# Kernel tuning notes

Measured on AMD Instinct MI355X. Metric: run time of the kernel, lower is better.

Reference implementation:

```python
import jax, jax.numpy as jnp
import numpy as np

BS, NQ, NV, E = 8, 1000, 20000, 256
HH, DH, L, P, FFN = 8, 32, 1, 4, 512
SPATIAL = ((100, 200),)  # (H, W) per level; sum(H*W) == NV


def layer_norm(x, w, b):
    mu = jnp.mean(x, -1, keepdims=True)
    var = jnp.mean((x - mu) ** 2, -1, keepdims=True)
    return (x - mu) / jnp.sqrt(var + 1e-5) * w + b


def mha(q_in, k_in, v_in, in_w, in_b, out_w, out_b):
    # q_in/k_in/v_in: (len, BS, E), batch_first=False semantics of nn.MultiheadAttention
    Wq, Wk, Wv = jnp.split(in_w, 3, axis=0)
    bq, bk, bv = jnp.split(in_b, 3, axis=0)
    def heads(x, W, b):  # (len,B,E) -> (B,HH,len,DH)
        y = x @ W.T + b
        return y.reshape(y.shape[0], BS, HH, DH).transpose(1, 2, 0, 3)
    q = heads(q_in, Wq, bq) / jnp.sqrt(jnp.asarray(DH, q_in.dtype))
    k = heads(k_in, Wk, bk)
    v = heads(v_in, Wv, bv)
    attn = jax.nn.softmax(jnp.einsum('bhqd,bhkd->bhqk', q, k), axis=-1)
    o = jnp.einsum('bhqk,bhkd->bhqd', attn, v)  # (B,HH,Lq,DH)
    o = o.transpose(2, 0, 1, 3).reshape(-1, BS, E)
    return o @ out_w.T + out_b


def bilinear_sample(img, grid):
    # img: (B,H,W,C); grid: (B,NQ,P,2) in [-1,1]; align_corners=False, zero padding
    B, H, W, C = img.shape
    x = (grid[..., 0] + 1.0) * 0.5 * W - 0.5
    y = (grid[..., 1] + 1.0) * 0.5 * H - 0.5
    x0 = jnp.floor(x); y0 = jnp.floor(y)
    wx = x - x0; wy = y - y0
    flat = img.reshape(B, H * W, C)
    def gather(xi, yi):
        valid = (xi >= 0) & (xi < W) & (yi >= 0) & (yi < H)
        xc = jnp.clip(xi, 0, W - 1).astype(jnp.int32)
        yc = jnp.clip(yi, 0, H - 1).astype(jnp.int32)
        idx = (yc * W + xc).reshape(B, -1, 1)
        v = jnp.take_along_axis(flat, idx, axis=1).reshape(*xi.shape, C)
        return v * valid[..., None].astype(img.dtype)
    v00 = gather(x0, y0); v01 = gather(x0 + 1, y0)
    v10 = gather(x0, y0 + 1); v11 = gather(x0 + 1, y0 + 1)
    wx = wx[..., None]; wy = wy[..., None]
    return (v00 * (1 - wx) * (1 - wy) + v01 * wx * (1 - wy)
            + v10 * (1 - wx) * wy + v11 * wx * wy)


def msda(value, sampling_locations, attention_weights):
    # value: (BS,NV,HH,DH); locations: (BS,NQ,HH,L,P,2); weights: (BS,NQ,HH,L,P)
    grids = 2.0 * sampling_locations - 1.0
    start = 0
    outs = []
    for lvl, (H, W) in enumerate(SPATIAL):
        v = value[:, start:start + H * W]           # (BS,HW,HH,DH)
        start += H * W
        img = v.transpose(0, 2, 1, 3).reshape(BS * HH, H, W, DH)
        g = grids[:, :, :, lvl].transpose(0, 2, 1, 3, 4).reshape(BS * HH, NQ, P, 2)
        outs.append(bilinear_sample(img, g))        # (BS*HH,NQ,P,DH)
    sampled = jnp.stack(outs, axis=2)               # (BS*HH,NQ,L,P,DH)
    aw = attention_weights.transpose(0, 2, 1, 3, 4).reshape(BS * HH, NQ, L, P)
    out = jnp.einsum('bqlpd,bqlp->bqd', sampled, aw)
    return out.reshape(BS, HH, NQ, DH).transpose(0, 2, 1, 3).reshape(BS, NQ, E)


def setup_inputs() -> dict:
    key = jax.random.key(0)
    ks = jax.random.split(key, 24)
    s = 1.0 / np.sqrt(E)
    # sampling_offsets bias: torch init grid (circular directions scaled by point idx)
    th = np.arange(HH, dtype=np.float32) * (2.0 * np.pi / HH)
    grid = np.stack([np.cos(th), np.sin(th)], -1)
    grid = grid / np.abs(grid).max(-1, keepdims=True)
    grid = np.tile(grid[:, None, None, :], (1, L, P, 1)) * np.arange(1, P + 1, dtype=np.float32)[None, None, :, None]
    return {
        'query': jax.random.normal(ks[0], (NQ, BS, E), jnp.float32),
        'query_pos': jax.random.normal(ks[1], (NQ, BS, E), jnp.float32),
        'value': jax.random.normal(ks[2], (NV, BS, E), jnp.float32),
        'reference_points': jax.random.uniform(ks[3], (BS, NQ, L, 2), jnp.float32),
        'in_proj_w': jax.random.normal(ks[4], (3 * E, E), jnp.float32) * s,
        'in_proj_b': jnp.zeros((3 * E,), jnp.float32),
        'out_proj_w': jax.random.normal(ks[5], (E, E), jnp.float32) * s,
        'out_proj_b': jnp.zeros((E,), jnp.float32),
        'ln1_w': jnp.ones((E,), jnp.float32), 'ln1_b': jnp.zeros((E,), jnp.float32),
        'ln2_w': jnp.ones((E,), jnp.float32), 'ln2_b': jnp.zeros((E,), jnp.float32),
        'ln3_w': jnp.ones((E,), jnp.float32), 'ln3_b': jnp.zeros((E,), jnp.float32),
        'off_w': jax.random.normal(ks[6], (HH * L * P * 2, E), jnp.float32) * 0.01,
        'off_b': jnp.asarray(grid.reshape(-1)),
        'aw_w': jax.random.normal(ks[7], (HH * L * P, E), jnp.float32) * 0.01,
        'aw_b': jnp.zeros((HH * L * P,), jnp.float32),
        'vproj_w': jax.random.normal(ks[8], (E, E), jnp.float32) * s,
        'vproj_b': jnp.zeros((E,), jnp.float32),
        'oproj_w': jax.random.normal(ks[9], (E, E), jnp.float32) * s,
        'oproj_b': jnp.zeros((E,), jnp.float32),
        'ffn_w1': jax.random.normal(ks[10], (FFN, E), jnp.float32) * s,
        'ffn_b1': jnp.zeros((FFN,), jnp.float32),
        'ffn_w2': jax.random.normal(ks[11], (E, FFN), jnp.float32) / np.sqrt(FFN),
        'ffn_b2': jnp.zeros((E,), jnp.float32),
    }


def reference(query, query_pos, value, reference_points,
              in_proj_w, in_proj_b, out_proj_w, out_proj_b,
              ln1_w, ln1_b, ln2_w, ln2_b, ln3_w, ln3_b,
              off_w, off_b, aw_w, aw_b, vproj_w, vproj_b, oproj_w, oproj_b,
              ffn_w1, ffn_b1, ffn_w2, ffn_b2):
    # --- self-attn: q=k=query+pos, v=query; residual inside; dropout=eval (identity)
    qp = query + query_pos
    x = layer_norm(query + mha(qp, qp, query, in_proj_w, in_proj_b, out_proj_w, out_proj_b), ln1_w, ln1_b)
    # --- deformable cross-attn ---
    xq_b = (x + query_pos).transpose(1, 0, 2)         # (BS,NQ,E)
    v = (value.transpose(1, 0, 2) @ vproj_w.T + vproj_b).reshape(BS, NV, HH, DH)
    off = (xq_b @ off_w.T + off_b).reshape(BS, NQ, HH, L, P, 2)
    aw = jax.nn.softmax((xq_b @ aw_w.T + aw_b).reshape(BS, NQ, HH, L * P), -1).reshape(BS, NQ, HH, L, P)
    norm = jnp.asarray([[w, h] for (h, w) in SPATIAL], jnp.float32)  # (L,2) = (W,H)
    loc = reference_points[:, :, None, :, None, :] + off / norm[None, None, None, :, None, :]
    ms = msda(v, loc, aw) @ oproj_w.T + oproj_b       # (BS,NQ,E)
    x = layer_norm(x + ms.transpose(1, 0, 2), ln2_w, ln2_b)
    # --- FFN ---
    h = jnp.maximum(x @ ffn_w1.T + ffn_b1, 0.0)
    return layer_norm(x + h @ ffn_w2.T + ffn_b2, ln3_w, ln3_b)
```

## Files before the change

### kernel.cpp

```cpp
#include <hip/hip_runtime.h>
#include <hip/hip_bf16.h>
#include <cmath>

constexpr int cBS = 8;
constexpr int cNQ = 1000;
constexpr int cNV = 20000;
constexpr int cE  = 256;
constexpr int cHH = 8;
constexpr int cDH = 32;
constexpr int cP  = 4;
constexpr int cFFN = 512;
constexpr int cH = 100;
constexpr int cW = 200;
constexpr int NTOK = cNQ * cBS;
constexpr size_t QKSZ2 = (size_t)64 * 1024 * cDH;

typedef float f32x4 __attribute__((ext_vector_type(4)));
typedef short bf16x8 __attribute__((ext_vector_type(8)));
union U8 { uint u[4]; bf16x8 v; };

__device__ __forceinline__ void split_bf(float x, ushort& h, ushort& l) {
    __hip_bfloat16 hb = __float2bfloat16(x);
    float hf = __bfloat162float(hb);
    __hip_bfloat16 lb = __float2bfloat16(x - hf);
    h = *reinterpret_cast<ushort*>(&hb);
    l = *reinterpret_cast<ushort*>(&lb);
}
__device__ __forceinline__ void pk_split2(float a, float b, uint& h, uint& l) {
    __hip_bfloat16 ah = __float2bfloat16(a), bh = __float2bfloat16(b);
    float arf = a - __bfloat162float(ah), brf = b - __bfloat162float(bh);
    __hip_bfloat16 al = __float2bfloat16(arf), bl = __float2bfloat16(brf);
    h = ((uint)*reinterpret_cast<ushort*>(&bh) << 16) | *reinterpret_cast<ushort*>(&ah);
    l = ((uint)*reinterpret_cast<ushort*>(&bl) << 16) | *reinterpret_cast<ushort*>(&al);
}

__global__ __launch_bounds__(256) void k_zerou4(uint4* __restrict__ p, int n)
{
    int i = blockIdx.x * 256 + threadIdx.x;
    if (i < n) p[i] = uint4{0u, 0u, 0u, 0u};
}

__global__ __launch_bounds__(256) void k_prepw(
    const float* __restrict__ Wsrc, ushort* __restrict__ wpk,
    int nkk , int total , int losz )
{
    int gid = blockIdx.x * 256 + threadIdx.x;
    if (gid >= total) return;
    int g  = gid & 3;
    int kk = (gid >> 2) % nkk;
    int n  = gid / (4 * nkk);
    const float* src = Wsrc + (size_t)n * (nkk * 32) + kk * 32 + 4 * g;
    float4 x0 = *reinterpret_cast<const float4*>(src);
    float4 x1 = *reinterpret_cast<const float4*>(src + 16);
    float xs[8] = {x0.x, x0.y, x0.z, x0.w, x1.x, x1.y, x1.z, x1.w};
    union { ushort s[8]; uint4 q; } hi_, lo_;
#pragma unroll
    for (int j = 0; j < 8; j++) split_bf(xs[j], hi_.s[j], lo_.s[j]);
    *reinterpret_cast<uint4*>(wpk + (size_t)gid * 8)        = hi_.q;
    *reinterpret_cast<uint4*>(wpk + losz + (size_t)gid * 8) = lo_.q;
}

__global__ __launch_bounds__(256) void k_prepw2(
    const float* __restrict__ Wsrc, ushort* __restrict__ wpk)
{
    int gid = blockIdx.x * 256 + threadIdx.x;
    if (gid >= 8192) return;
    int lane = gid & 63;
    int kk   = (gid >> 6) & 7;
    int nblk = gid >> 9;
    int ln = lane & 15, g = lane >> 4;
    const float* src = Wsrc + (size_t)(nblk * 16 + ln) * cE + kk * 32 + 4 * g;
    float4 x0 = *reinterpret_cast<const float4*>(src);
    float4 x1 = *reinterpret_cast<const float4*>(src + 16);
    float xs[8] = {x0.x, x0.y, x0.z, x0.w, x1.x, x1.y, x1.z, x1.w};
    union { ushort s[8]; uint4 q; } hi_, lo_;
#pragma unroll
    for (int j = 0; j < 8; j++) split_bf(xs[j], hi_.s[j], lo_.s[j]);
    *reinterpret_cast<uint4*>(wpk + (size_t)gid * 8)         = hi_.q;
    *reinterpret_cast<uint4*>(wpk + 65536 + (size_t)gid * 8) = lo_.q;
}

__global__ __launch_bounds__(256) void k_bgemm2(
    const float* __restrict__ A, const ushort* __restrict__ wpk2,
    const float* __restrict__ bias, float* __restrict__ vimg)
{
    __shared__ float lds[64][36];
    const int t    = threadIdx.x;
    const int w    = t >> 6;
    const int lane = t & 63;
    const int g    = lane >> 4;
    const int ln   = lane & 15;
    const int bm   = blockIdx.x * 64;
    const ushort* wlo = wpk2 + 65536;

    f32x4 acc[4][4];
#pragma unroll
    for (int mt = 0; mt < 4; mt++)
#pragma unroll
        for (int nt = 0; nt < 4; nt++) acc[mt][nt] = {0.f, 0.f, 0.f, 0.f};

    const int srow = t >> 2;
    const int scg  = (t & 3) * 8;

    for (int kk = 0; kk < 8; kk++) {
        {
            const float* src = A + (size_t)(bm + srow) * cE + kk * 32 + scg;
            float4 u0 = *reinterpret_cast<const float4*>(src);
            float4 u1 = *reinterpret_cast<const float4*>(src + 4);
            *reinterpret_cast<float4*>(&lds[srow][scg])     = u0;
            *reinterpret_cast<float4*>(&lds[srow][scg + 4]) = u1;
        }
        __syncthreads();

        U8 wh[4], wl[4];
#pragma unroll
        for (int nt = 0; nt < 4; nt++) {
            size_t off = (((size_t)(w * 4 + nt) * 8 + kk) * 64 + lane) * 8;
            *reinterpret_cast<uint4*>(&wh[nt].u[0]) = *reinterpret_cast<const uint4*>(wpk2 + off);
            *reinterpret_cast<uint4*>(&wl[nt].u[0]) = *reinterpret_cast<const uint4*>(wlo + off);
        }

#pragma unroll
        for (int mt = 0; mt < 4; mt++) {
            int row = mt * 16 + ln;
            float4 x0 = *reinterpret_cast<const float4*>(&lds[row][4 * g]);
            float4 x1 = *reinterpret_cast<const float4*>(&lds[row][16 + 4 * g]);
            float xs[8] = {x0.x, x0.y, x0.z, x0.w, x1.x, x1.y, x1.z, x1.w};
            U8 aH, aL;
            union { ushort s[8]; uint u[4]; } hs, ls;
#pragma unroll
            for (int j = 0; j < 8; j++) split_bf(xs[j], hs.s[j], ls.s[j]);
#pragma unroll
            for (int i = 0; i < 4; i++) { aH.u[i] = hs.u[i]; aL.u[i] = ls.u[i]; }
#pragma unroll
            for (int nt = 0; nt < 4; nt++) {
                acc[mt][nt] = __builtin_amdgcn_mfma_f32_16x16x32_bf16(aL.v, wh[nt].v, acc[mt][nt], 0, 0, 0);
                acc[mt][nt] = __builtin_amdgcn_mfma_f32_16x16x32_bf16(aH.v, wl[nt].v, acc[mt][nt], 0, 0, 0);
                acc[mt][nt] = __builtin_amdgcn_mfma_f32_16x16x32_bf16(aH.v, wh[nt].v, acc[mt][nt], 0, 0, 0);
            }
        }
        __syncthreads();
    }

#pragma unroll
    for (int nt = 0; nt < 4; nt++) {
        int n = w * 64 + nt * 16 + ln;
        float bv = bias[n];
#pragma unroll
        for (int mt = 0; mt < 4; mt++) {
#pragma unroll
            for (int r = 0; r < 4; r++) {
                int gr = bm + mt * 16 + 4 * g + r;
                vimg[(size_t)gr * cE + n] = acc[mt][nt][r] + bv;
            }
        }
    }
}

__global__ __launch_bounds__(256) void k_oagemm(
    const float* __restrict__ xq, const ushort* __restrict__ wpk,
    float* __restrict__ raw)
{
    const int w    = threadIdx.x >> 6;
    const int lane = threadIdx.x & 63;
    const int g    = lane >> 4;
    const int ln   = lane & 15;
    const int row0 = blockIdx.x * 64 + w * 16;
    const ushort* wlo = wpk + 24576;

    f32x4 acc[6];
#pragma unroll
    for (int nt = 0; nt < 6; nt++) acc[nt] = {0.f, 0.f, 0.f, 0.f};

    for (int kk = 0; kk < 8; kk++) {
        const float* ap = xq + (size_t)(row0 + ln) * cE + kk * 32 + 4 * g;
        float4 u0 = *reinterpret_cast<const float4*>(ap);
        float4 u1 = *reinterpret_cast<const float4*>(ap + 16);
        float xs[8] = {u0.x, u0.y, u0.z, u0.w, u1.x, u1.y, u1.z, u1.w};
        U8 aH, aL;
        union { ushort s[8]; uint u[4]; } hs, ls;
#pragma unroll
        for (int j = 0; j < 8; j++) split_bf(xs[j], hs.s[j], ls.s[j]);
#pragma unroll
        for (int i = 0; i < 4; i++) { aH.u[i] = hs.u[i]; aL.u[i] = ls.u[i]; }
#pragma unroll
        for (int nt = 0; nt < 6; nt++) {
            int n = nt * 16 + ln;
            size_t off = ((size_t)(n * 8 + kk) * 4 + g) * 8;
            U8 wh, wl;
            *reinterpret_cast<uint4*>(&wh.u[0]) = *reinterpret_cast<const uint4*>(wpk + off);
            *reinterpret_cast<uint4*>(&wl.u[0]) = *reinterpret_cast<const uint4*>(wlo + off);
            acc[nt] = __builtin_amdgcn_mfma_f32_16x16x32_bf16(aL.v, wh.v, acc[nt], 0, 0, 0);
            acc[nt] = __builtin_amdgcn_mfma_f32_16x16x32_bf16(aH.v, wl.v, acc[nt], 0, 0, 0);
            acc[nt] = __builtin_amdgcn_mfma_f32_16x16x32_bf16(aH.v, wh.v, acc[nt], 0, 0, 0);
        }
    }

#pragma unroll
    for (int nt = 0; nt < 6; nt++) {
        int n = nt * 16 + ln;
#pragma unroll
        for (int r = 0; r < 4; r++) {
            int row = row0 + 4 * g + r;
            raw[(size_t)row * 96 + n] = acc[nt][r];
        }
    }
}

__global__ __launch_bounds__(256) void k_locaw(
    const float* __restrict__ raw, const float* __restrict__ offb,
    const float* __restrict__ awbias, const float* __restrict__ refp,
    float* __restrict__ locO, float* __restrict__ awO)
{
    int gid = blockIdx.x * 256 + threadIdx.x;
    if (gid >= NTOK * 96) return;
    int i = gid % 96;
    int tok = gid / 96;
    int q = tok >> 3, b = tok & 7;
    int bq = b * cNQ + q;
    const float* rr = raw + (size_t)tok * 96;
    if (i < 64) {
        int c = i & 1;
        float offv = rr[i] + offb[i];
        float refv = refp[((size_t)b * cNQ + q) * 2 + c];
        float nrm = (c == 0) ? 200.f : 100.f;
        locO[(size_t)bq * 64 + i] = refv + offv / nrm;
    } else {
        int j = i - 64;
        int gbase = j & ~3;
        float x0 = rr[64 + gbase + 0] + awbias[gbase + 0];
        float x1 = rr[64 + gbase + 1] + awbias[gbase + 1];
        float x2 = rr[64 + gbase + 2] + awbias[gbase + 2];
        float x3 = rr[64 + gbase + 3] + awbias[gbase + 3];
        float xm = rr[64 + j] + awbias[j];
        float mx = fmaxf(fmaxf(x0, x1), fmaxf(x2, x3));
        float e = __expf(xm - mx);
        float ssum = __expf(x0 - mx) + __expf(x1 - mx) + __expf(x2 - mx) + __expf(x3 - mx);
        awO[(size_t)bq * 32 + j] = e / ssum;
    }
}

constexpr int MM_QKV   = 1;
constexpr int MM_PLAIN = 2;
constexpr int MM_RELU  = 3;
constexpr int MM_OPROJ = 4;

template <int MODE, int TKK, int NFULL>
__global__ __launch_bounds__(256) void k_mgemm(
    const float* __restrict__ A, const float* __restrict__ A2,
    const ushort* __restrict__ wpk, int losz,
    const float* __restrict__ bias,
    void* __restrict__ C0, void* __restrict__ C1, void* __restrict__ C2)
{
    const int w    = threadIdx.x >> 6;
    const int lane = threadIdx.x & 63;
    const int g    = lane >> 4;
    const int ln   = lane & 15;
    const int bm   = blockIdx.x * 32;
    const int slab = blockIdx.y;
    const int nb   = slab * 256 + w * 64;
    const ushort* wlo = wpk + losz;
    const int K = TKK * 32;

    f32x4 acc[2][4];
#pragma unroll
    for (int mt = 0; mt < 2; mt++)
#pragma unroll
        for (int nt = 0; nt < 4; nt++) acc[mt][nt] = {0.f, 0.f, 0.f, 0.f};

    U8 wh[2][4], wl[2][4];
    float ax[2][2][8];

#define MG_LOADW(kk, buf) {                                                        \
    _Pragma("unroll")                                                              \
    for (int nt = 0; nt < 4; nt++) {                                               \
        int n = nb + nt * 16 + ln;                                                 \
        size_t off = ((size_t)(n * TKK + (kk)) * 4 + g) * 8;                       \
        *reinterpret_cast<uint4*>(&wh[buf][nt].u[0]) = *reinterpret_cast<const uint4*>(wpk + off); \
        *reinterpret_cast<uint4*>(&wl[buf][nt].u[0]) = *reinterpret_cast<const uint4*>(wlo + off); \
    } }

#define MG_LOADA(kk, buf) {                                                        \
    _Pragma("unroll")                                                              \
    for (int mt = 0; mt < 2; mt++) {                                               \
        const float* ap = A + (size_t)(bm + mt * 16 + ln) * K + (kk) * 32 + 4 * g; \
        float4 u0 = *reinterpret_cast<const float4*>(ap);                          \
        float4 u1 = *reinterpret_cast<const float4*>(ap + 16);                     \
        if (MODE == MM_QKV && slab < 2) {                                          \
            const float* bp = A2 + (size_t)(bm + mt * 16 + ln) * K + (kk) * 32 + 4 * g; \
            float4 v0 = *reinterpret_cast<const float4*>(bp);                      \
            float4 v1 = *reinterpret_cast<const float4*>(bp + 16);                 \
            u0.x += v0.x; u0.y += v0.y; u0.z += v0.z; u0.w += v0.w;                \
            u1.x += v1.x; u1.y += v1.y; u1.z += v1.z; u1.w += v1.w;                \
        }                                                                          \
        ax[buf][mt][0] = u0.x; ax[buf][mt][1] = u0.y;                              \
        ax[buf][mt][2] = u0.z; ax[buf][mt][3] = u0.w;                              \
        ax[buf][mt][4] = u1.x; ax[buf][mt][5] = u1.y;                              \
        ax[buf][mt][6] = u1.z; ax[buf][mt][7] = u1.w;                              \
    } }

#define MG_STEP(buf) {                                                             \
    _Pragma("unroll")                                                              \
    for (int mt = 0; mt < 2; mt++) {                                               \
        U8 aH, aL;                                                                 \
        union { ushort s[8]; uint u[4]; } hs, ls;                                  \
        _Pragma("unroll")                                                          \
        for (int j = 0; j < 8; j++) split_bf(ax[buf][mt][j], hs.s[j], ls.s[j]);    \
        _Pragma("unroll")                                                          \
        for (int i = 0; i < 4; i++) { aH.u[i] = hs.u[i]; aL.u[i] = ls.u[i]; }      \
        _Pragma("unroll")                                                          \
        for (int nt = 0; nt < 4; nt++) {                                           \
            acc[mt][nt] = __builtin_amdgcn_mfma_f32_16x16x32_bf16(aL.v, wh[buf][nt].v, acc[mt][nt], 0, 0, 0); \
            acc[mt][nt] = __builtin_amdgcn_mfma_f32_16x16x32_bf16(aH.v, wl[buf][nt].v, acc[mt][nt], 0, 0, 0); \
            acc[mt][nt] = __builtin_amdgcn_mfma_f32_16x16x32_bf16(aH.v, wh[buf][nt].v, acc[mt][nt], 0, 0, 0); \
        }                                                                          \
    } }

    MG_LOADW(0, 0)
    MG_LOADA(0, 0)
#pragma unroll
    for (int kk = 0; kk < TKK; kk++) {
        if (kk + 1 < TKK) {
            MG_LOADW(kk + 1, (kk + 1) & 1)
            MG_LOADA(kk + 1, (kk + 1) & 1)
        }
        MG_STEP(kk & 1)
    }
#undef MG_LOADW
#undef MG_LOADA
#undef MG_STEP

#pragma unroll
    for (int nt = 0; nt < 4; nt++) {
        int n = nb + nt * 16 + ln;
        float bv = bias[n];
#pragma unroll
        for (int mt = 0; mt < 2; mt++) {
#pragma unroll
            for (int r = 0; r < 4; r++) {
                int gr = bm + mt * 16 + 4 * g + r;
                float val = acc[mt][nt][r] + bv;
                if (MODE == MM_QKV) {
                    int tok = gr >> 3, b = gr & 7;
                    int nloc = n & 255, h = nloc >> 5, d = nloc & 31;
                    if (slab == 0) val *= 0.17677669529663687f;
                    ushort hs, ls;
                    split_bf(val, hs, ls);
                    if (slab < 2) {
                        int slot = ((d >> 2) & 3) * 8 + (d & 3) + 4 * (d >> 4);
                        ushort* base = (slab == 0) ? (ushort*)C0 : (ushort*)C1;
                        size_t off = ((size_t)(b * cHH + h) * 1024 + tok) * 32 + slot;
                        base[off]         = hs;
                        base[QKSZ2 + off] = ls;
                    } else {
                        int o = tok & 31, kbi = tok >> 5;
                        int slot = ((o >> 2) & 3) * 8 + (o & 3) + 4 * (o >> 4);
                        ushort* vb = (ushort*)C2;
                        size_t off = ((size_t)(b * cHH + h) * 32 + d) * 1024 + kbi * 32 + slot;
                        vb[off]         = hs;
                        vb[QKSZ2 + off] = ls;
                    }
                } else if (MODE == MM_OPROJ) {
                    int b = gr / cNQ, q = gr - b * cNQ;
                    ((float*)C0)[((size_t)q * cBS + b) * cE + n] = val;
                } else {
                    if (MODE == MM_RELU) val = fmaxf(val, 0.f);
                    ((float*)C0)[(size_t)gr * NFULL + n] = val;
                }
            }
        }
    }
}

__global__ __launch_bounds__(256) void k_attn3(
    const ushort* __restrict__ qhi, const ushort* __restrict__ qlo,
    const ushort* __restrict__ khi, const ushort* __restrict__ klo,
    const ushort* __restrict__ vhi, const ushort* __restrict__ vlo,
    float* __restrict__ po, float* __restrict__ plsum)
{
    const int bid   = blockIdx.x;
    const int xcd   = bid & 7;
    const int inner = bid >> 3;
    const int bh    = ((inner & 7) << 3) + xcd;
    const int rest  = inner >> 3;
    const int qbix  = rest & 7;
    const int z     = rest >> 3;

    const int w    = threadIdx.x >> 6;
    const int lane = threadIdx.x & 63;
    const int g    = lane >> 4;
    const int ql   = lane & 15;
    const int qA   = qbix * 128 + w * 32;

    const size_t qoffA = ((size_t)bh * 1024 + qA + ql) * 32 + g * 8;
    U8 bQAh, bQAl, bQBh, bQBl;
    *reinterpret_cast<uint4*>(&bQAh.u[0]) = *reinterpret_cast<const uint4*>(qhi + qoffA);
    *reinterpret_cast<uint4*>(&bQAl.u[0]) = *reinterpret_cast<const uint4*>(qlo + qoffA);
    *reinterpret_cast<uint4*>(&bQBh.u[0]) = *reinterpret_cast<const uint4*>(qhi + qoffA + 16 * 32);
    *reinterpret_cast<uint4*>(&bQBl.u[0]) = *reinterpret_cast<const uint4*>(qlo + qoffA + 16 * 32);
    const size_t koff = ((size_t)bh * 1024 + ql) * 32 + g * 8;
    const size_t voff = ((size_t)bh * 32 + ql) * 1024 + g * 8;

    f32x4 oA0 = {0.f,0.f,0.f,0.f}, oA1 = {0.f,0.f,0.f,0.f};
    f32x4 oB0 = {0.f,0.f,0.f,0.f}, oB1 = {0.f,0.f,0.f,0.f};
    float lpartA = 0.f, lpartB = 0.f;
    const f32x4 zz = {0.f, 0.f, 0.f, 0.f};

    const int kt0 = z * 16;
#pragma unroll
    for (int kti = 0; kti < 16; kti++) {
        const int kt = kt0 + kti;
        U8 k0h, k1h, k0l, k1l, v0h, v1h, v0l, v1l;
        {
            size_t kb32 = (size_t)kt * 32 * 32;
            *reinterpret_cast<uint4*>(&k0h.u[0]) = *reinterpret_cast<const uint4*>(khi + koff + kb32);
            *reinterpret_cast<uint4*>(&k1h.u[0]) = *reinterpret_cast<const uint4*>(khi + koff + kb32 + 512);
            *reinterpret_cast<uint4*>(&k0l.u[0]) = *reinterpret_cast<const uint4*>(klo + koff + kb32);
            *reinterpret_cast<uint4*>(&k1l.u[0]) = *reinterpret_cast<const uint4*>(klo + koff + kb32 + 512);
            size_t vb32 = voff + (size_t)kt * 32;
            *reinterpret_cast<uint4*>(&v0h.u[0]) = *reinterpret_cast<const uint4*>(vhi + vb32);
            *reinterpret_cast<uint4*>(&v1h.u[0]) = *reinterpret_cast<const uint4*>(vhi + vb32 + 16 * 1024);
            *reinterpret_cast<uint4*>(&v0l.u[0]) = *reinterpret_cast<const uint4*>(vlo + vb32);
            *reinterpret_cast<uint4*>(&v1l.u[0]) = *reinterpret_cast<const uint4*>(vlo + vb32 + 16 * 1024);
        }

        const bool tail = (kti == 15) && (z == 1);

        f32x4 sA0 = __builtin_amdgcn_mfma_f32_16x16x32_bf16(k0l.v, bQAh.v, zz, 0, 0, 0);
        sA0 = __builtin_amdgcn_mfma_f32_16x16x32_bf16(k0h.v, bQAl.v, sA0, 0, 0, 0);
        sA0 = __builtin_amdgcn_mfma_f32_16x16x32_bf16(k0h.v, bQAh.v, sA0, 0, 0, 0);
        f32x4 sB0 = __builtin_amdgcn_mfma_f32_16x16x32_bf16(k0l.v, bQBh.v, zz, 0, 0, 0);
        sB0 = __builtin_amdgcn_mfma_f32_16x16x32_bf16(k0h.v, bQBl.v, sB0, 0, 0, 0);
        sB0 = __builtin_amdgcn_mfma_f32_16x16x32_bf16(k0h.v, bQBh.v, sB0, 0, 0, 0);
        f32x4 sA1, sB1;
        if (tail) {
            int tb = 31 * 32 + 4 * g;
#pragma unroll
            for (int r = 0; r < 4; r++) {
                if (tb + r >= cNQ) { sA0[r] = -INFINITY; sB0[r] = -INFINITY; }
            }
            sA1[0] = sA1[1] = sA1[2] = sA1[3] = -INFINITY;
            sB1[0] = sB1[1] = sB1[2] = sB1[3] = -INFINITY;
        } else {
            sA1 = __builtin_amdgcn_mfma_f32_16x16x32_bf16(k1l.v, bQAh.v, zz, 0, 0, 0);
            sA1 = __builtin_amdgcn_mfma_f32_16x16x32_bf16(k1h.v, bQAl.v, sA1, 0, 0, 0);
            sA1 = __builtin_amdgcn_mfma_f32_16x16x32_bf16(k1h.v, bQAh.v, sA1, 0, 0, 0);
            sB1 = __builtin_amdgcn_mfma_f32_16x16x32_bf16(k1l.v, bQBh.v, zz, 0, 0, 0);
            sB1 = __builtin_amdgcn_mfma_f32_16x16x32_bf16(k1h.v, bQBl.v, sB1, 0, 0, 0);
            sB1 = __builtin_amdgcn_mfma_f32_16x16x32_bf16(k1h.v, bQBh.v, sB1, 0, 0, 0);
        }

        float pA00 = __expf(sA0[0]), pA01 = __expf(sA0[1]);
        float pA02 = __expf(sA0[2]), pA03 = __expf(sA0[3]);
        float pA10 = __expf(sA1[0]), pA11 = __expf(sA1[1]);
        float pA12 = __expf(sA1[2]), pA13 = __expf(sA1[3]);
        lpartA += ((pA00 + pA01) + (pA02 + pA03)) + ((pA10 + pA11) + (pA12 + pA13));
        float pB00 = __expf(sB0[0]), pB01 = __expf(sB0[1]);
        float pB02 = __expf(sB0[2]), pB03 = __expf(sB0[3]);
        float pB10 = __expf(sB1[0]), pB11 = __expf(sB1[1]);
        float pB12 = __expf(sB1[2]), pB13 = __expf(sB1[3]);
        lpartB += ((pB00 + pB01) + (pB02 + pB03)) + ((pB10 + pB11) + (pB12 + pB13));

        U8 fpAh, fpAl, fpBh, fpBl;
        pk_split2(pA00, pA01, fpAh.u[0], fpAl.u[0]);
        pk_split2(pA02, pA03, fpAh.u[1], fpAl.u[1]);
        pk_split2(pA10, pA11, fpAh.u[2], fpAl.u[2]);
        pk_split2(pA12, pA13, fpAh.u[3], fpAl.u[3]);
        pk_split2(pB00, pB01, fpBh.u[0], fpBl.u[0]);
        pk_split2(pB02, pB03, fpBh.u[1], fpBl.u[1]);
        pk_split2(pB10, pB11, fpBh.u[2], fpBl.u[2]);
        pk_split2(pB12, pB13, fpBh.u[3], fpBl.u[3]);

        oA0 = __builtin_amdgcn_mfma_f32_16x16x32_bf16(v0l.v, fpAh.v, oA0, 0, 0, 0);
        oA0 = __builtin_amdgcn_mfma_f32_16x16x32_bf16(v0h.v, fpAl.v, oA0, 0, 0, 0);
        oA0 = __builtin_amdgcn_mfma_f32_16x16x32_bf16(v0h.v, fpAh.v, oA0, 0, 0, 0);
        oA1 = __builtin_amdgcn_mfma_f32_16x16x32_bf16(v1l.v, fpAh.v, oA1, 0, 0, 0);
        oA1 = __builtin_amdgcn_mfma_f32_16x16x32_bf16(v1h.v, fpAl.v, oA1, 0, 0, 0);
        oA1 = __builtin_amdgcn_mfma_f32_16x16x32_bf16(v1h.v, fpAh.v, oA1, 0, 0, 0);
        oB0 = __builtin_amdgcn_mfma_f32_16x16x32_bf16(v0l.v, fpBh.v, oB0, 0, 0, 0);
        oB0 = __builtin_amdgcn_mfma_f32_16x16x32_bf16(v0h.v, fpBl.v, oB0, 0, 0, 0);
        oB0 = __builtin_amdgcn_mfma_f32_16x16x32_bf16(v0h.v, fpBh.v, oB0, 0, 0, 0);
        oB1 = __builtin_amdgcn_mfma_f32_16x16x32_bf16(v1l.v, fpBh.v, oB1, 0, 0, 0);
        oB1 = __builtin_amdgcn_mfma_f32_16x16x32_bf16(v1h.v, fpBl.v, oB1, 0, 0, 0);
        oB1 = __builtin_amdgcn_mfma_f32_16x16x32_bf16(v1h.v, fpBh.v, oB1, 0, 0, 0);
    }

    float lsumA = lpartA;
    lsumA += __shfl_xor(lsumA, 16, 64);
    lsumA += __shfl_xor(lsumA, 32, 64);
    float lsumB = lpartB;
    lsumB += __shfl_xor(lsumB, 16, 64);
    lsumB += __shfl_xor(lsumB, 32, 64);

    {
        const int q = qA + ql;
        if (q < cNQ) {
            size_t base = ((size_t)(z * 64 + bh) * 1000 + q) * 32;
            float4 v0, v1;
            v0.x = oA0[0]; v0.y = oA0[1]; v0.z = oA0[2]; v0.w = oA0[3];
            v1.x = oA1[0]; v1.y = oA1[1]; v1.z = oA1[2]; v1.w = oA1[3];
            *reinterpret_cast<float4*>(po + base + 4 * g)      = v0;
            *reinterpret_cast<float4*>(po + base + 16 + 4 * g) = v1;
            if (g == 0) plsum[(size_t)(z * 64 + bh) * 1000 + q] = lsumA;
        }
    }
    {
        const int q = qA + 16 + ql;
        if (q < cNQ) {
            size_t base = ((size_t)(z * 64 + bh) * 1000 + q) * 32;
            float4 v0, v1;
            v0.x = oB0[0]; v0.y = oB0[1]; v0.z = oB0[2]; v0.w = oB0[3];
            v1.x = oB1[0]; v1.y = oB1[1]; v1.z = oB1[2]; v1.w = oB1[3];
            *reinterpret_cast<float4*>(po + base + 4 * g)      = v0;
            *reinterpret_cast<float4*>(po + base + 16 + 4 * g) = v1;
            if (g == 0) plsum[(size_t)(z * 64 + bh) * 1000 + q] = lsumB;
        }
    }
}

__global__ __launch_bounds__(256) void k_ared(
    const float* __restrict__ po, const float* __restrict__ plsum,
    float* __restrict__ outp)
{
    int gid = blockIdx.x * 256 + threadIdx.x;
    if (gid >= 64 * 1000 * 32) return;
    int d   = gid & 31;
    int rem = gid >> 5;
    int q   = rem % 1000;
    int bh  = rem / 1000;
    float o = po[gid] + po[(size_t)64 * 1000 * 32 + gid];
    float l = plsum[rem] + plsum[64000 + rem];
    int b = bh >> 3, h = bh & 7;
    outp[((size_t)q * cBS + b) * cE + h * 32 + d] = o / l;
}

__global__ __launch_bounds__(256) void k_ln(
    const float* __restrict__ a, const float* __restrict__ b,
    const float* __restrict__ w, const float* __restrict__ bias,
    const float* __restrict__ addc,
    float* __restrict__ outp, float* __restrict__ out2)
{
    int rrow = blockIdx.x, t = threadIdx.x;
    size_t base = (size_t)rrow * cE;
    float v = a[base + t] + b[base + t];
    float s = v;
#pragma unroll
    for (int off = 32; off > 0; off >>= 1) s += __shfl_down(s, off, 64);
    __shared__ float red1[4], red2[4];
    int wid = t >> 6, lane = t & 63;
    if (lane == 0) red1[wid] = s;
    __syncthreads();
    float mu = (red1[0] + red1[1] + red1[2] + red1[3]) * (1.f / cE);
    float e = v - mu;
    float s2 = e * e;
#pragma unroll
    for (int off = 32; off > 0; off >>= 1) s2 += __shfl_down(s2, off, 64);
    if (lane == 0) red2[wid] = s2;
    __syncthreads();
    float var = (red2[0] + red2[1] + red2[2] + red2[3]) * (1.f / cE);
    float y = e * (1.f / sqrtf(var + 1e-5f)) * w[t] + bias[t];
    outp[base + t] = y;
    if (out2 != nullptr) out2[base + t] = y + addc[base + t];
}

__device__ __forceinline__ float samp_one(const float* __restrict__ img, int x, int y)
{
    bool ok = (x >= 0) & (x < cW) & (y >= 0) & (y < cH);
    int xc = min(max(x, 0), cW - 1);
    int yc = min(max(y, 0), cH - 1);
    float v = img[(size_t)(yc * cW + xc) * (cBS * cE)];
    return ok ? v : 0.f;
}

__global__ __launch_bounds__(256) void k_msda(
    const float* __restrict__ vimg, const float* __restrict__ loc,
    const float* __restrict__ aw, float* __restrict__ msp)
{
    int gid = blockIdx.x * 256 + threadIdx.x;
    int d  = gid & 31;
    int h  = (gid >> 5) & 7;
    int bq = gid >> 8;
    int b  = bq / cNQ;
    const float* lp = loc + ((size_t)bq * cHH + h) * (cP * 2);
    const float* ap = aw + ((size_t)bq * cHH + h) * cP;
    const float* img = vimg + (size_t)b * cE + h * cDH + d;
    float acc = 0.f;
#pragma unroll
    for (int p = 0; p < cP; p++) {
        float g0 = 2.f * lp[p * 2 + 0] - 1.f;
        float g1 = 2.f * lp[p * 2 + 1] - 1.f;
        float xf = (g0 + 1.f) * 0.5f * (float)cW - 0.5f;
        float yf = (g1 + 1.f) * 0.5f * (float)cH - 0.5f;
        float x0f = floorf(xf), y0f = floorf(yf);
        float wx = xf - x0f, wy = yf - y0f;
        int x0 = (int)x0f, y0 = (int)y0f;
        float v00 = samp_one(img, x0,     y0);
        float v01 = samp_one(img, x0 + 1, y0);
        float v10 = samp_one(img, x0,     y0 + 1);
        float v11 = samp_one(img, x0 + 1, y0 + 1);
        float bil = v00 * (1.f - wx) * (1.f - wy) + v01 * wx * (1.f - wy)
                  + v10 * (1.f - wx) * wy        + v11 * wx * wy;
        acc = fmaf(bil, ap[p], acc);
    }
    msp[gid] = acc;
}

extern "C" void kernel_launch(void* const* d_in, const int* in_sizes, int n_in,
                              void* d_out, int out_size, void* d_ws, size_t ws_size,
                              hipStream_t stream)
{
    const float* query = (const float*)d_in[0];
    const float* qpos  = (const float*)d_in[1];
    const float* value = (const float*)d_in[2];
    const float* refp  = (const float*)d_in[3];
    const float* inw   = (const float*)d_in[4];
    const float* inb   = (const float*)d_in[5];
    const float* outw  = (const float*)d_in[6];
    const float* outb  = (const float*)d_in[7];
    const float* ln1w  = (const float*)d_in[8];
    const float* ln1b  = (const float*)d_in[9];
    const float* ln2w  = (const float*)d_in[10];
    const float* ln2b  = (const float*)d_in[11];
    const float* ln3w  = (const float*)d_in[12];
    const float* ln3b  = (const float*)d_in[13];
    const float* offw  = (const float*)d_in[14];
    const float* offb  = (const float*)d_in[15];
    const float* aww   = (const float*)d_in[16];
    const float* awbias= (const float*)d_in[17];
    const float* vpw   = (const float*)d_in[18];
    const float* vpb   = (const float*)d_in[19];
    const float* opw   = (const float*)d_in[20];
    const float* opb   = (const float*)d_in[21];
    const float* f1w   = (const float*)d_in[22];
    const float* f1b   = (const float*)d_in[23];
    const float* f2w   = (const float*)d_in[24];
    const float* f2b   = (const float*)d_in[25];
    float* out = (float*)d_out;

    float* ws = (float*)d_ws;
    const size_t S = (size_t)NTOK * cE;
    const size_t BPADF = 6 * QKSZ2 / 2;
    const size_t WPKF = 655360 + 24576;
    const size_t PLS  = 128000;
    const size_t need = 2 * S + BPADF + 512000 + 256000 + WPKF + PLS + (size_t)cBS * cHH * cNV * cDH;
    if (ws_size < need * sizeof(float)) return;

    float* P0   = ws;
    float* P1   = ws + S;
    float* Bpad = ws + 2 * S;
    float* locb = Bpad + BPADF;
    float* awb2 = locb + 512000;
    float* wpkf = awb2 + 256000;
    float* plsb = wpkf + WPKF;
    float* vimg = plsb + PLS;

    ushort* qhi = (ushort*)Bpad;
    ushort* qlo = qhi + QKSZ2;
    ushort* khi = qhi + 2 * QKSZ2;
    ushort* klo = qhi + 3 * QKSZ2;
    ushort* vhi = qhi + 4 * QKSZ2;
    ushort* vlo = qhi + 5 * QKSZ2;

    ushort* wpk_vp = (ushort*)wpkf;
    ushort* wpk_in = wpk_vp + 131072;
    ushort* wpk_ou = wpk_in + 393216;
    ushort* wpk_op = wpk_ou + 131072;
    ushort* wpk_f1 = wpk_op + 131072;
    ushort* wpk_f2 = wpk_f1 + 262144;
    ushort* wpk_oa = wpk_f2 + 262144;

    k_prepw2<<<dim3(32), dim3(256), 0, stream>>>(vpw, wpk_vp);
    k_prepw<<<dim3(96), dim3(256), 0, stream>>>(inw,  wpk_in, 8,  24576, 196608);
    k_prepw<<<dim3(32), dim3(256), 0, stream>>>(outw, wpk_ou, 8,  8192,  65536);
    k_prepw<<<dim3(32), dim3(256), 0, stream>>>(opw,  wpk_op, 8,  8192,  65536);
    k_prepw<<<dim3(64), dim3(256), 0, stream>>>(f1w,  wpk_f1, 8,  16384, 131072);
    k_prepw<<<dim3(64), dim3(256), 0, stream>>>(f2w,  wpk_f2, 16, 16384, 131072);
    k_prepw<<<dim3(8),  dim3(256), 0, stream>>>(offw, wpk_oa, 8,  2048,  24576);
    k_prepw<<<dim3(4),  dim3(256), 0, stream>>>(aww,  wpk_oa + 16384, 8, 1024, 24576);

    k_bgemm2<<<dim3(2500), dim3(256), 0, stream>>>(value, wpk_vp, vpb, vimg);

    k_zerou4<<<dim3(2048), dim3(256), 0, stream>>>(
        reinterpret_cast<uint4*>(vhi), (int)(2 * QKSZ2 * 2 / 16));

    k_mgemm<MM_QKV, 8, 768><<<dim3(250, 3), dim3(256), 0, stream>>>(
        query, qpos, wpk_in, 196608, inb, qhi, khi, vhi);

    k_attn3<<<dim3(1024), dim3(256), 0, stream>>>(
        qhi, qlo, khi, klo, vhi, vlo, P0, plsb);

    float* attn_pre = Bpad;
    k_ared<<<dim3(8000), dim3(256), 0, stream>>>(P0, plsb, attn_pre);

    float* mha_y = P1;
    k_mgemm<MM_PLAIN, 8, 256><<<dim3(250, 1), dim3(256), 0, stream>>>(
        attn_pre, nullptr, wpk_ou, 65536, outb, mha_y, nullptr, nullptr);

    float* x  = Bpad;
    float* xq = Bpad + S;
    k_ln<<<dim3(NTOK), dim3(256), 0, stream>>>(query, mha_y, ln1w, ln1b, qpos, x, xq);

    float* rawb = P0;
    k_oagemm<<<dim3(125), dim3(256), 0, stream>>>(xq, wpk_oa, rawb);
    k_locaw<<<dim3((NTOK * 96 + 255) / 256), dim3(256), 0, stream>>>(
        rawb, offb, awbias, refp, locb, awb2);

    float* ms_pre = P1;
    k_msda<<<dim3(NTOK * cE / 256), dim3(256), 0, stream>>>(vimg, locb, awb2, ms_pre);

    float* ms_y = P0;
    k_mgemm<MM_OPROJ, 8, 256><<<dim3(250, 1), dim3(256), 0, stream>>>(
        ms_pre, nullptr, wpk_op, 65536, opb, ms_y, nullptr, nullptr);

    float* x2 = Bpad + 2 * S;
    k_ln<<<dim3(NTOK), dim3(256), 0, stream>>>(x, ms_y, ln2w, ln2b, nullptr, x2, nullptr);

    float* hbuf = Bpad;
    k_mgemm<MM_RELU, 8, 512><<<dim3(250, 2), dim3(256), 0, stream>>>(
        x2, nullptr, wpk_f1, 131072, f1b, hbuf, nullptr, nullptr);
    float* y3 = P0;
    k_mgemm<MM_PLAIN, 16, 256><<<dim3(250, 1), dim3(256), 0, stream>>>(
        hbuf, nullptr, wpk_f2, 131072, f2b, y3, nullptr, nullptr);

    k_ln<<<dim3(NTOK), dim3(256), 0, stream>>>(x2, y3, ln3w, ln3b, nullptr, out, nullptr);
}
```

Baseline: 423.8 us.

## Double-buffer value-projection GEMM A tiles via direct global-to-LDS loads with XOR swizzle

The value-projection GEMM now stages A tiles into two LDS buffers using global_load_lds (direct global-to-LDS DMA), so the next k-slice is prefetched while the current one is consumed. The padded row layout is replaced by an XOR-swizzled 128-byte row layout to avoid bank conflicts, and the k-loop is fully unrolled. This aims to hide global load latency and skip the register round trip, but it relies on correct wave-uniform LDS base addressing for the builtin and uses twice the LDS.

```diff
diff --git a/kernel.cpp b/kernel.cpp
--- a/kernel.cpp
+++ b/kernel.cpp
@@ -34,6 +34,13 @@
     l = ((uint)*reinterpret_cast<ushort*>(&bl) << 16) | *reinterpret_cast<ushort*>(&al);
 }
 
+__device__ __forceinline__ void gl_lds16(const float* g, float* l) {
+    __builtin_amdgcn_global_load_lds(
+        (const __attribute__((address_space(1))) unsigned int*)g,
+        (__attribute__((address_space(3))) unsigned int*)l,
+        16, 0, 0);
+}
+
 __global__ __launch_bounds__(256) void k_zerou4(uint4* __restrict__ p, int n)
 {
     int i = blockIdx.x * 256 + threadIdx.x;
@@ -84,7 +91,7 @@
     const float* __restrict__ A, const ushort* __restrict__ wpk2,
     const float* __restrict__ bias, float* __restrict__ vimg)
 {
-    __shared__ float lds[64][36];
+    __shared__ float lds[2][2048];
     const int t    = threadIdx.x;
     const int w    = t >> 6;
     const int lane = t & 63;
@@ -99,18 +106,24 @@
 #pragma unroll
         for (int nt = 0; nt < 4; nt++) acc[mt][nt] = {0.f, 0.f, 0.f, 0.f};
 
-    const int srow = t >> 2;
-    const int scg  = (t & 3) * 8;
-
+#define VSTAGE(buf, kkv) {                                                          \
+    int row0_ = (w << 4) + (lane >> 3);                                             \
+    int c0_ = ((lane & 7) << 4) ^ ((row0_ & 7) << 4);                               \
+    gl_lds16(A + (size_t)(bm + row0_) * cE + (kkv) * 32 + (c0_ >> 2),               \
+             &lds[buf][(w << 9)]);                                                  \
+    int row1_ = row0_ + 8;                                                          \
+    int c1_ = ((lane & 7) << 4) ^ ((row1_ & 7) << 4);                               \
+    gl_lds16(A + (size_t)(bm + row1_) * cE + (kkv) * 32 + (c1_ >> 2),               \
+             &lds[buf][(w << 9) + 256]);                                            \
+}
+
+    VSTAGE(0, 0)
+    __syncthreads();
+
+#pragma unroll
     for (int kk = 0; kk < 8; kk++) {
-        {
-            const float* src = A + (size_t)(bm + srow) * cE + kk * 32 + scg;
-            float4 u0 = *reinterpret_cast<const float4*>(src);
-            float4 u1 = *reinterpret_cast<const float4*>(src + 4);
-            *reinterpret_cast<float4*>(&lds[srow][scg])     = u0;
-            *reinterpret_cast<float4*>(&lds[srow][scg + 4]) = u1;
-        }
-        __syncthreads();
+        const int cur = kk & 1;
+        if (kk < 7) VSTAGE(cur ^ 1, kk + 1)
 
         U8 wh[4], wl[4];
 #pragma unroll
@@ -120,11 +133,13 @@
             *reinterpret_cast<uint4*>(&wl[nt].u[0]) = *reinterpret_cast<const uint4*>(wlo + off);
         }
 
+        const char* lb = (const char*)(&lds[cur][0]);
 #pragma unroll
         for (int mt = 0; mt < 4; mt++) {
             int row = mt * 16 + ln;
-            float4 x0 = *reinterpret_cast<const float4*>(&lds[row][4 * g]);
-            float4 x1 = *reinterpret_cast<const float4*>(&lds[row][16 + 4 * g]);
+            int mk = (row & 7) << 4;
+            float4 x0 = *reinterpret_cast<const float4*>(lb + row * 128 + ((g * 16) ^ mk));
+            float4 x1 = *reinterpret_cast<const float4*>(lb + row * 128 + ((64 + g * 16) ^ mk));
             float xs[8] = {x0.x, x0.y, x0.z, x0.w, x1.x, x1.y, x1.z, x1.w};
             U8 aH, aL;
             union { ushort s[8]; uint u[4]; } hs, ls;
@@ -141,6 +156,7 @@
         }
         __syncthreads();
     }
+#undef VSTAGE
 
 #pragma unroll
     for (int nt = 0; nt < 4; nt++) {
```

Result: faster. 412.5 us (-2.7%).
